# Kernel optimization log

Hardware: AMD Instinct MI355X
Metric: run time of the kernel (lower is better)

The kernel has to match this reference:

```python
import jax, jax.numpy as jnp
import numpy as np

DIM = 1024
B, L = 4, 4096


def setup_inputs() -> dict:
    key = jax.random.key(0)
    ks = jax.random.split(key, 6)
    s = 1.0 / np.sqrt(DIM)
    x = jax.random.normal(ks[0], (B, L, DIM), dtype=jnp.float32)
    Wk = jax.random.uniform(ks[1], (DIM, DIM), jnp.float32, -s, s)
    bk = jax.random.uniform(ks[2], (DIM,), jnp.float32, -s, s)
    Wv = jax.random.uniform(ks[3], (DIM, DIM), jnp.float32, -s, s)
    bv = jax.random.uniform(ks[4], (DIM,), jnp.float32, -s, s)
    ln_g = jnp.ones((DIM,), jnp.float32)
    ln_b = jnp.zeros((DIM,), jnp.float32)
    Wo = jax.random.uniform(ks[5], (DIM, DIM), jnp.float32, -s, s)
    bo = jnp.zeros((DIM,), jnp.float32)
    return {"x": x, "Wk": Wk, "bk": bk, "Wv": Wv, "bv": bv,
            "ln_g": ln_g, "ln_b": ln_b, "Wo": Wo, "bo": bo}


def reference(x, Wk, bk, Wv, bv, ln_g, ln_b, Wo, bo):
    B_, L_, D = x.shape
    # key/value projections (torch Linear: x @ W.T + b)
    keys = x @ Wk.T + bk
    keys = keys / jnp.maximum(jnp.linalg.norm(keys, axis=-1, keepdims=True), 1e-12)
    values = x @ Wv.T + bv
    # circular convolution via FFT: bind keys with values
    Kf = jnp.fft.rfft(keys, axis=-1)
    Vf = jnp.fft.rfft(values, axis=-1)
    bound = jnp.fft.irfft(Kf * Vf, n=D, axis=-1)
    # cumulative holographic memory over sequence
    memory = jnp.cumsum(bound, axis=1)
    # circular correlation (unbind): conj of key spectrum
    Mf = jnp.fft.rfft(memory, axis=-1)
    retrieved = jnp.fft.irfft(Mf * jnp.conj(Kf), n=D, axis=-1)
    # position-dependent normalization: sqrt(1..L)
    norm = jnp.sqrt(jnp.arange(1, L_ + 1, dtype=x.dtype)).reshape(1, L_, 1)
    r = retrieved / norm
    # LayerNorm (eps=1e-5) + output Linear
    mu = jnp.mean(r, axis=-1, keepdims=True)
    var = jnp.var(r, axis=-1, keepdims=True)
    r_ln = (r - mu) * jax.lax.rsqrt(var + 1e-5) * ln_g + ln_b
    return x + (r_ln @ Wo.T + bo)
```

## Files before the change

### kernel.cpp

```cpp
#include <hip/hip_runtime.h>
#include <math.h>

#define B_SZ 4
#define L_SZ 4096
#define D_SZ 1024
#define M_SZ (B_SZ * L_SZ)
#define NBINS 513
#define CCH   (2 * NBINS)
#define TLEN 8
#define NCH  (L_SZ / TLEN)
#define NG   32

typedef short bf16x8 __attribute__((ext_vector_type(8)));
typedef float f32x4  __attribute__((ext_vector_type(4)));
typedef unsigned short us8 __attribute__((ext_vector_type(8)));

#define AS1 __attribute__((address_space(1)))
#define AS3 __attribute__((address_space(3)))

__device__ inline unsigned short f2bf(float f) {
    unsigned int u = __float_as_uint(f);
    u += 0x7fffu + ((u >> 16) & 1u);
    return (unsigned short)(u >> 16);
}

__global__ __launch_bounds__(256) void cast_f32_bf16(
        const float* __restrict__ in, unsigned short* __restrict__ out, int n8) {
    int i = blockIdx.x * 256 + threadIdx.x;
    if (i >= n8) return;
    const float4* p = (const float4*)in + 2 * (size_t)i;
    float4 a = p[0], b = p[1];
    us8 o;
    o[0] = f2bf(a.x); o[1] = f2bf(a.y); o[2] = f2bf(a.z); o[3] = f2bf(a.w);
    o[4] = f2bf(b.x); o[5] = f2bf(b.y); o[6] = f2bf(b.z); o[7] = f2bf(b.w);
    *(us8*)(out + (size_t)i * 8) = o;
}

__global__ __launch_bounds__(256) void cast_w3(
        const float* __restrict__ Wk, const float* __restrict__ Wv,
        const float* __restrict__ Wo,
        unsigned short* __restrict__ WB, unsigned short* __restrict__ Wob, int n8) {
    int i = blockIdx.x * 256 + threadIdx.x;
    if (i >= n8) return;
    const int which = blockIdx.y;
    const float* src = (which == 0) ? Wk : (which == 1) ? Wv : Wo;
    unsigned short* dst = (which == 0) ? WB : (which == 1) ? (WB + D_SZ * D_SZ) : Wob;
    const float4* p = (const float4*)src + 2 * (size_t)i;
    float4 a = p[0], b = p[1];
    us8 o;
    o[0] = f2bf(a.x); o[1] = f2bf(a.y); o[2] = f2bf(a.z); o[3] = f2bf(a.w);
    o[4] = f2bf(b.x); o[5] = f2bf(b.y); o[6] = f2bf(b.z); o[7] = f2bf(b.w);
    *(us8*)(dst + (size_t)i * 8) = o;
}

template<int CNT>
__global__ __launch_bounds__(512, 4) void gemm_mfma(
        const unsigned short* __restrict__ A, const unsigned short* __restrict__ W,
        const float* __restrict__ bias0, const float* __restrict__ bias1,
        const float* __restrict__ resid,
        float* __restrict__ C0, float* __restrict__ C1, int M, int K) {
    __shared__ unsigned short Abuf[3][256 * 32];
    __shared__ unsigned short Bbuf[3][128 * 32];
    const int id   = blockIdx.x;
    const int bx   = (id >> 3) % CNT;
    const int by   = (id & 7) + 8 * (id / (8 * CNT));
    const int tid  = threadIdx.x;
    const int lane = tid & 63;
    const int wid  = tid >> 6;
    const int wr   = wid >> 2;
    const int wc   = wid & 3;
    const int bm   = by * 256;
    const int bn   = bx * 128;

    const int sl = tid >> 3;
    const int sq = (tid & 7) ^ (sl & 7);
    const int srow = 2 * sl + (sq >> 2);
    const int skof = (sq & 3) * 8;
    const unsigned short* Abase = A + (size_t)(bm + srow) * K + skof;
    const unsigned short* Wbase = W + (size_t)(bn + srow) * K + skof;
    const int dstoff = tid * 16;

    auto stage3 = [&](int slot, int kk) {
        __builtin_amdgcn_global_load_lds((const AS1 unsigned int*)(Abase + kk),
            (AS3 unsigned int*)((char*)&Abuf[slot][0] + dstoff), 16, 0, 0);
        __builtin_amdgcn_global_load_lds((const AS1 unsigned int*)(Abase + (size_t)128 * K + kk),
            (AS3 unsigned int*)((char*)&Abuf[slot][128 * 32] + dstoff), 16, 0, 0);
        __builtin_amdgcn_global_load_lds((const AS1 unsigned int*)(Wbase + kk),
            (AS3 unsigned int*)((char*)&Bbuf[slot][0] + dstoff), 16, 0, 0);
    };

    const int fr = lane & 15;
    const int kq = lane >> 4;
    const int rslot = (((((fr & 1) << 2) + kq) ^ ((fr >> 1) & 7)) << 4);
    const int aoff0 = wr * 8192 + (fr >> 1) * 128 + rslot;
    const int boff0 = wc * 2048 + (fr >> 1) * 128 + rslot;

    f32x4 acc[8][2] = {};

    const int nt = K >> 5;
    stage3(0, 0);
    stage3(1, 32);
    asm volatile("s_waitcnt vmcnt(3)" ::: "memory");
    __builtin_amdgcn_s_barrier();
    asm volatile("" ::: "memory");

    int slot = 0, slot2 = 2;
    for (int cur = 0; cur < nt; ++cur) {
        bf16x8 a[8], b[2];
        const char* Ab = (const char*)&Abuf[slot][0];
        const char* Bb = (const char*)&Bbuf[slot][0];
        #pragma unroll
        for (int nf = 0; nf < 2; nf++)
            b[nf] = *(const bf16x8*)(Bb + boff0 + nf * 1024);
        #pragma unroll
        for (int mf = 0; mf < 8; mf++)
            a[mf] = *(const bf16x8*)(Ab + aoff0 + mf * 1024);
        if (cur + 2 < nt) stage3(slot2, (cur + 2) << 5);
        __builtin_amdgcn_s_setprio(1);
        #pragma unroll
        for (int mf = 0; mf < 8; mf++)
            #pragma unroll
            for (int nf = 0; nf < 2; nf++)
                acc[mf][nf] = __builtin_amdgcn_mfma_f32_16x16x32_bf16(
                                  a[mf], b[nf], acc[mf][nf], 0, 0, 0);
        __builtin_amdgcn_s_setprio(0);
        if (cur + 2 < nt) { asm volatile("s_waitcnt vmcnt(3)" ::: "memory"); }
        else              { asm volatile("s_waitcnt vmcnt(0)" ::: "memory"); }
        __builtin_amdgcn_s_barrier();
        asm volatile("" ::: "memory");
        slot  = (slot  == 2) ? 0 : slot  + 1;
        slot2 = (slot2 == 2) ? 0 : slot2 + 1;
    }

    const int col0 = lane & 15;
    const int quad = lane >> 4;
    #pragma unroll
    for (int nf = 0; nf < 2; nf++) {
        const int ng = bn + wc * 32 + nf * 16 + col0;
        const int half = ng >> 10;
        const int n = ng & 1023;
        float* __restrict__ Cp = half ? C1 : C0;
        const float bv = half ? bias1[n] : bias0[n];
        #pragma unroll
        for (int mf = 0; mf < 8; mf++) {
            #pragma unroll
            for (int r = 0; r < 4; r++) {
                const int m = bm + wr * 128 + mf * 16 + quad * 4 + r;
                float v = acc[mf][nf][r] + bv;
                size_t off = (size_t)m * 1024 + n;
                if (resid) v += resid[off];
                Cp[off] = v;
            }
        }
    }
}

#define SWZ(a) ((a) ^ (((a) >> 4) & 15))

struct cplx { float r, i; };
__device__ inline cplx cmul(cplx a, cplx b) {
    return {a.r * b.r - a.i * b.i, a.r * b.i + a.i * b.r};
}

__device__ inline void r4bfly(cplx v[4], float s) {
    cplx t0 {v[0].r + v[2].r, v[0].i + v[2].i};
    cplx t1 {v[0].r - v[2].r, v[0].i - v[2].i};
    cplx t2 {v[1].r + v[3].r, v[1].i + v[3].i};
    cplx t3 {v[1].r - v[3].r, v[1].i - v[3].i};
    cplx j3 {-s * t3.i, s * t3.r};
    v[0] = {t0.r + t2.r, t0.i + t2.i};
    v[2] = {t0.r - t2.r, t0.i - t2.i};
    v[1] = {t1.r + j3.r, t1.i + j3.i};
    v[3] = {t1.r - j3.r, t1.i - j3.i};
}

template<int SIGN>
__device__ inline void make_w1(cplx w1s[4], int tid) {
    const float s = (float)SIGN;
    #pragma unroll
    for (int q = 1; q <= 3; q++) {
        const int Ls = 1 << (2 * q);
        const float ang = s * 1.57079632679489662f * (float)(tid & (Ls - 1)) / (float)Ls;
        float sn, cs; __sincosf(ang, &sn, &cs);
        w1s[q - 1] = {cs, sn};
    }
    float sn, cs;
    __sincosf(s * 1.57079632679489662f * (float)tid / 256.0f, &sn, &cs);
    w1s[3] = {cs, sn};
}

template<int SIGN>
__device__ inline void fft1024_tw(float2* bA, float2* bB, cplx v[4], int tid,
                                  const cplx w1s[4]) {
    const float s = (float)SIGN;
    r4bfly(v, s);
    {
        const int base = tid << 2;
        #pragma unroll
        for (int e = 0; e < 4; e++)
            bA[SWZ(base + e)] = make_float2(v[e].r, v[e].i);
    }
    __syncthreads();
    float2* cur = bA;
    float2* nxt = bB;
    #pragma unroll
    for (int q = 1; q <= 3; q++) {
        const int Ls = 1 << (2 * q);
        #pragma unroll
        for (int k = 0; k < 4; k++) {
            float2 t = cur[SWZ(tid + (k << 8))];
            v[k] = {t.x, t.y};
        }
        const int d = tid & (Ls - 1);
        cplx w1 = w1s[q - 1];
        cplx w2 = cmul(w1, w1);
        cplx w3 = cmul(w2, w1);
        v[1] = cmul(v[1], w1);
        v[2] = cmul(v[2], w2);
        v[3] = cmul(v[3], w3);
        r4bfly(v, s);
        const int base = ((tid >> (2 * q)) << (2 * q + 2)) + d;
        #pragma unroll
        for (int e = 0; e < 4; e++)
            nxt[SWZ(base + (e << (2 * q)))] = make_float2(v[e].r, v[e].i);
        float2* tmp = cur; cur = nxt; nxt = tmp;
        __syncthreads();
    }
    #pragma unroll
    for (int k = 0; k < 4; k++) {
        float2 t = cur[SWZ(tid + (k << 8))];
        v[k] = {t.x, t.y};
    }
    {
        cplx w1 = w1s[3];
        cplx w2 = cmul(w1, w1);
        cplx w3 = cmul(w2, w1);
        v[1] = cmul(v[1], w1);
        v[2] = cmul(v[2], w2);
        v[3] = cmul(v[3], w3);
        r4bfly(v, s);
    }
}

__global__ __launch_bounds__(256) void bind_cum_kernel(
        float* __restrict__ KIO, const float* __restrict__ V,
        float* __restrict__ P, float* __restrict__ totals) {
    __shared__ float2 bA[1024], bB[1024];
    __shared__ float red[4];
    const int blk = blockIdx.x;
    const int tid = threadIdx.x;
    const int wv  = tid >> 6;
    const int ln  = tid & 63;
    const size_t tok0 = (size_t)blk * TLEN;

    cplx w1s[4];
    make_w1<-1>(w1s, tid);

    float r0r = 0.f, r0i = 0.f, r1r = 0.f, r1i = 0.f, r2r = 0.f, r2i = 0.f;

    float kvC[4], vvC[4];
    {
        const float* krow = KIO + tok0 * D_SZ;
        const float* vrow = V   + tok0 * D_SZ;
        #pragma unroll
        for (int k = 0; k < 4; k++) {
            kvC[k] = krow[tid + (k << 8)];
            vvC[k] = vrow[tid + (k << 8)];
        }
    }

    for (int tk = 0; tk < TLEN; ++tk) {
        const size_t token = tok0 + tk;
        float* krow = KIO + token * D_SZ;

        float ss = 0.f;
        #pragma unroll
        for (int k = 0; k < 4; k++) ss += kvC[k] * kvC[k];
        #pragma unroll
        for (int m = 1; m < 64; m <<= 1) ss += __shfl_xor(ss, m, 64);
        if (ln == 0) red[wv] = ss;
        __syncthreads();
        const float scale = 1.0f /
            fmaxf(sqrtf(red[0] + red[1] + red[2] + red[3]), 1e-12f);

        cplx z[4];
        #pragma unroll
        for (int k = 0; k < 4; k++) z[k] = {kvC[k] * scale, vvC[k]};

        if (tk + 1 < TLEN) {
            const float* krowN = KIO + (token + 1) * D_SZ;
            const float* vrowN = V   + (token + 1) * D_SZ;
            #pragma unroll
            for (int k = 0; k < 4; k++) {
                kvC[k] = krowN[tid + (k << 8)];
                vvC[k] = vrowN[tid + (k << 8)];
            }
        }

        fft1024_tw<-1>(bA, bB, z, tid, w1s);

        #pragma unroll
        for (int e = 0; e < 4; e++)
            bA[SWZ(tid + (e << 8))] = make_float2(z[e].r, z[e].i);
        __syncthreads();

        float2* Po = (float2*)(P + token * CCH);
        auto procbin = [&](int bin, float& rr, float& ri) {
            float2 Zb = bA[SWZ(bin)];
            float2 Zm = bA[SWZ((1024 - bin) & 1023)];
            float ar = 0.5f * (Zb.x + Zm.x);
            float ai = 0.5f * (Zb.y - Zm.y);
            float br = 0.5f * (Zb.y + Zm.y);
            float bi = 0.5f * (Zm.x - Zb.x);
            rr += ar * br - ai * bi;
            ri += ar * bi + ai * br;
            Po[bin] = make_float2(rr, ri);
            if (bin == 0)        krow[0] = ar;
            else if (bin == 512) krow[1] = ar;
            else { krow[2 * bin] = ar; krow[2 * bin + 1] = ai; }
        };
        procbin(tid,       r0r, r0i);
        procbin(tid + 256, r1r, r1i);
        if (tid == 0) procbin(512, r2r, r2i);
    }

    float* trow = totals + (size_t)blk * CCH;
    trow[2 * tid]             = r0r;  trow[2 * tid + 1]         = r0i;
    trow[2 * (tid + 256)]     = r1r;  trow[2 * (tid + 256) + 1] = r1i;
    if (tid == 0) { trow[1024] = r2r; trow[1025] = r2i; }
}

__global__ __launch_bounds__(256) void scan_s1(
        float* __restrict__ totals, float* __restrict__ gt) {
    const int c = blockIdx.x * 256 + threadIdx.x;
    if (c >= CCH) return;
    const int g = blockIdx.y;
    const int b = blockIdx.z;
    float run = 0.f;
    #pragma unroll
    for (int i = 0; i < 16; i++) {
        size_t idx = ((size_t)(b * NCH + g * 16 + i)) * CCH + c;
        float v = totals[idx];
        totals[idx] = run;
        run += v;
    }
    gt[((size_t)(b * NG + g)) * CCH + c] = run;
}

__global__ __launch_bounds__(256) void scan_s2(float* __restrict__ gt) {
    const int c = blockIdx.x * 256 + threadIdx.x;
    if (c >= CCH) return;
    const int b = blockIdx.y;
    float run = 0.f;
    #pragma unroll
    for (int g = 0; g < NG; g++) {
        size_t idx = ((size_t)(b * NG + g)) * CCH + c;
        float v = gt[idx];
        gt[idx] = run;
        run += v;
    }
}

__global__ __launch_bounds__(256) void unbind4_ln_kernel(
        const float* __restrict__ P, const float* __restrict__ totals,
        const float* __restrict__ gt, const float* __restrict__ KF,
        const float* __restrict__ ln_g, const float* __restrict__ ln_b,
        unsigned short* __restrict__ RLNb) {
    __shared__ float2 bA[1024], bB[1024];
    __shared__ float2 offsh[NBINS];
    __shared__ float red[16];
    const int blk = blockIdx.x;
    const int tid = threadIdx.x;
    const int wv  = tid >> 6;
    const int ln  = tid & 63;
    const size_t tok0 = (size_t)blk * TLEN;
    const int bidx  = (int)(tok0 >> 12);
    const int t0    = (int)(tok0 & (L_SZ - 1));
    const int chunk = t0 >> 3;

    {
        const float2* off2 = (const float2*)(totals + (size_t)(bidx * NCH + chunk) * CCH);
        const float2* gof2 = (const float2*)(gt + (size_t)(bidx * NG + (chunk >> 4)) * CCH);
        auto ldo = [&](int bin) {
            float2 o = off2[bin], g = gof2[bin];
            offsh[bin] = make_float2(o.x + g.x, o.y + g.y);
        };
        ldo(tid); ldo(tid + 256);
        if (tid == 0) ldo(512);
    }

    cplx w1s[4];
    make_w1<1>(w1s, tid);

    float gv[4], bev[4];
    #pragma unroll
    for (int e = 0; e < 4; e++) {
        gv[e]  = ln_g[tid + (e << 8)];
        bev[e] = ln_b[tid + (e << 8)];
    }
    __syncthreads();

    for (int p = 0; p < 4; ++p) {
        const size_t ta = tok0 + 2 * p, tb = ta + 1;
        const float2* Sa2 = (const float2*)(P + ta * CCH);
        const float2* Sb2 = (const float2*)(P + tb * CCH);
        const float*  Ka  = KF + ta * D_SZ;
        const float*  Kb  = KF + tb * D_SZ;

        auto zc = [&](int bin, const float2* S2, const float* kf, float2 og) {
            float kr, ki;
            if (bin == 0)        { kr = kf[0]; ki = 0.f; }
            else if (bin == 512) { kr = kf[1]; ki = 0.f; }
            else { float2 k2 = *(const float2*)(kf + 2 * bin); kr = k2.x; ki = k2.y; }
            float2 s2 = S2[bin];
            float sr = s2.x + og.x, si = s2.y + og.y;
            return make_float2(sr * kr + si * ki, si * kr - sr * ki);
        };
        auto fill = [&](int bin) {
            float2 og = offsh[bin];
            float2 Za = zc(bin, Sa2, Ka, og);
            float2 Zb = zc(bin, Sb2, Kb, og);
            bA[SWZ(bin)] = make_float2(Za.x - Zb.y, Za.y + Zb.x);
            if (bin != 0 && bin != 512)
                bA[SWZ(1024 - bin)] = make_float2(Za.x + Zb.y, Zb.x - Za.y);
        };
        fill(tid);
        fill(tid + 256);
        if (tid == 0) fill(512);
        __syncthreads();

        cplx z[4];
        #pragma unroll
        for (int k = 0; k < 4; k++) {
            float2 c = bA[SWZ(tid + (k << 8))];
            z[k] = {c.x, c.y};
        }
        __syncthreads();
        fft1024_tw<1>(bA, bB, z, tid, w1s);

        const int t_a = t0 + 2 * p;
        const float sa = (1.0f / 1024.0f) * rsqrtf((float)(t_a + 1));
        const float sb = (1.0f / 1024.0f) * rsqrtf((float)(t_a + 2));
        float ra[4], rb[4];
        float s1a = 0.f, s2a = 0.f, s1b = 0.f, s2b = 0.f;
        #pragma unroll
        for (int e = 0; e < 4; e++) {
            ra[e] = z[e].r * sa;
            rb[e] = z[e].i * sb;
            s1a += ra[e]; s2a += ra[e] * ra[e];
            s1b += rb[e]; s2b += rb[e] * rb[e];
        }
        #pragma unroll
        for (int m = 1; m < 64; m <<= 1) {
            s1a += __shfl_xor(s1a, m, 64);
            s2a += __shfl_xor(s2a, m, 64);
            s1b += __shfl_xor(s1b, m, 64);
            s2b += __shfl_xor(s2b, m, 64);
        }
        if (ln == 0) {
            red[wv] = s1a; red[4 + wv] = s2a; red[8 + wv] = s1b; red[12 + wv] = s2b;
        }
        __syncthreads();
        const float S1a = red[0] + red[1] + red[2] + red[3];
        const float S2a = red[4] + red[5] + red[6] + red[7];
        const float S1b = red[8] + red[9] + red[10] + red[11];
        const float S2b = red[12] + red[13] + red[14] + red[15];
        const float mua = S1a * (1.0f / 1024.0f);
        const float vara = S2a * (1.0f / 1024.0f) - mua * mua;
        const float rsa = rsqrtf(vara + 1e-5f);
        const float mub = S1b * (1.0f / 1024.0f);
        const float varb = S2b * (1.0f / 1024.0f) - mub * mub;
        const float rsb = rsqrtf(varb + 1e-5f);

        unsigned short* outA = RLNb + ta * D_SZ;
        unsigned short* outB = RLNb + tb * D_SZ;
        #pragma unroll
        for (int e = 0; e < 4; e++) {
            const int d = tid + (e << 8);
            outA[d] = f2bf((ra[e] - mua) * rsa * gv[e] + bev[e]);
            outB[d] = f2bf((rb[e] - mub) * rsb * gv[e] + bev[e]);
        }
        __syncthreads();
    }
}

extern "C" void kernel_launch(void* const* d_in, const int* in_sizes, int n_in,
                              void* d_out, int out_size, void* d_ws, size_t ws_size,
                              hipStream_t stream) {
    (void)in_sizes; (void)n_in; (void)out_size; (void)ws_size;
    const float* x    = (const float*)d_in[0];
    const float* Wk   = (const float*)d_in[1];
    const float* bk   = (const float*)d_in[2];
    const float* Wv   = (const float*)d_in[3];
    const float* bv   = (const float*)d_in[4];
    const float* ln_g = (const float*)d_in[5];
    const float* ln_b = (const float*)d_in[6];
    const float* Wo   = (const float*)d_in[7];
    const float* bo   = (const float*)d_in[8];
    float* out = (float*)d_out;

    char* w = (char*)d_ws;
    float* Kraw   = (float*)w;  w += (size_t)M_SZ * D_SZ * 4;
    float* V      = (float*)w;  w += (size_t)M_SZ * D_SZ * 4;
    float* P      = (float*)w;  w += (size_t)M_SZ * CCH * 4;
    unsigned short* xb  = (unsigned short*)w;  w += (size_t)M_SZ * D_SZ * 2;
    unsigned short* WB  = (unsigned short*)w;  w += (size_t)2 * D_SZ * D_SZ * 2;
    unsigned short* Wob = (unsigned short*)w;  w += (size_t)D_SZ * D_SZ * 2;
    unsigned short* RLNb = (unsigned short*)V;
    float* totals = (float*)xb;
    float* gt     = (float*)xb + (size_t)B_SZ * NCH * CCH;

    const int n8x = M_SZ * D_SZ / 8;
    const int n8w = D_SZ * D_SZ / 8;
    cast_f32_bf16<<<n8x / 256, 256, 0, stream>>>(x, xb, n8x);
    dim3 wgrid(n8w / 256, 3);
    cast_w3<<<wgrid, 256, 0, stream>>>(Wk, Wv, Wo, WB, Wob, n8w);

    gemm_mfma<16><<<(M_SZ / 256) * 16, 512, 0, stream>>>(
        xb, WB, bk, bv, nullptr, Kraw, V, M_SZ, D_SZ);

    bind_cum_kernel<<<M_SZ / TLEN, 256, 0, stream>>>(Kraw, V, P, totals);

    dim3 g1((CCH + 255) / 256, NG, B_SZ);
    scan_s1<<<g1, 256, 0, stream>>>(totals, gt);
    dim3 g2((CCH + 255) / 256, B_SZ);
    scan_s2<<<g2, 256, 0, stream>>>(gt);

    unbind4_ln_kernel<<<M_SZ / TLEN, 256, 0, stream>>>(
        P, totals, gt, Kraw, ln_g, ln_b, RLNb);

    gemm_mfma<8><<<(M_SZ / 256) * 8, 512, 0, stream>>>(
        RLNb, Wob, bo, bo, x, out, out, M_SZ, D_SZ);
}
```

Before: 391.2 us.

## Store K/V projections and partial spectra intermediates in bf16

The projection GEMM now writes K and V in bf16 rather than fp32. The bind kernel reads them as bf16 and writes its partial-sum spectra P and the key spectra in bf16, and the unbind kernel reads them back as bf16. This roughly halves the global-memory traffic between the GEMM, bind and unbind stages. In exchange, precision drops in the intermediates, including the prefix-sum partials, which can raise numerical error.

```diff
diff --git a/kernel.cpp b/kernel.cpp
--- a/kernel.cpp
+++ b/kernel.cpp
@@ -22,6 +22,9 @@
     unsigned int u = __float_as_uint(f);
     u += 0x7fffu + ((u >> 16) & 1u);
     return (unsigned short)(u >> 16);
+}
+__device__ inline float bf2f(unsigned short u) {
+    return __uint_as_float(((unsigned int)u) << 16);
 }
 
 __global__ __launch_bounds__(256) void cast_f32_bf16(
@@ -53,12 +56,12 @@
     *(us8*)(dst + (size_t)i * 8) = o;
 }
 
-template<int CNT>
+template<int CNT, bool OBF16>
 __global__ __launch_bounds__(512, 4) void gemm_mfma(
         const unsigned short* __restrict__ A, const unsigned short* __restrict__ W,
         const float* __restrict__ bias0, const float* __restrict__ bias1,
         const float* __restrict__ resid,
-        float* __restrict__ C0, float* __restrict__ C1, int M, int K) {
+        void* __restrict__ C0v, void* __restrict__ C1v, int M, int K) {
     __shared__ unsigned short Abuf[3][256 * 32];
     __shared__ unsigned short Bbuf[3][128 * 32];
     const int id   = blockIdx.x;
@@ -139,8 +142,8 @@
         const int ng = bn + wc * 32 + nf * 16 + col0;
         const int half = ng >> 10;
         const int n = ng & 1023;
-        float* __restrict__ Cp = half ? C1 : C0;
         const float bv = half ? bias1[n] : bias0[n];
+        void* Cv = half ? C1v : C0v;
         #pragma unroll
         for (int mf = 0; mf < 8; mf++) {
             #pragma unroll
@@ -148,8 +151,12 @@
                 const int m = bm + wr * 128 + mf * 16 + quad * 4 + r;
                 float v = acc[mf][nf][r] + bv;
                 size_t off = (size_t)m * 1024 + n;
-                if (resid) v += resid[off];
-                Cp[off] = v;
+                if constexpr (OBF16) {
+                    ((unsigned short*)Cv)[off] = f2bf(v);
+                } else {
+                    if (resid) v += resid[off];
+                    ((float*)Cv)[off] = v;
+                }
             }
         }
     }
@@ -243,8 +250,8 @@
 }
 
 __global__ __launch_bounds__(256) void bind_cum_kernel(
-        float* __restrict__ KIO, const float* __restrict__ V,
-        float* __restrict__ P, float* __restrict__ totals) {
+        unsigned short* __restrict__ KIO, const unsigned short* __restrict__ Vb,
+        unsigned short* __restrict__ P, float* __restrict__ totals) {
     __shared__ float2 bA[1024], bB[1024];
     __shared__ float red[4];
     const int blk = blockIdx.x;
@@ -260,18 +267,18 @@
 
     float kvC[4], vvC[4];
     {
-        const float* krow = KIO + tok0 * D_SZ;
-        const float* vrow = V   + tok0 * D_SZ;
+        const unsigned short* krow = KIO + tok0 * D_SZ;
+        const unsigned short* vrow = Vb  + tok0 * D_SZ;
         #pragma unroll
         for (int k = 0; k < 4; k++) {
-            kvC[k] = krow[tid + (k << 8)];
-            vvC[k] = vrow[tid + (k << 8)];
+            kvC[k] = bf2f(krow[tid + (k << 8)]);
+            vvC[k] = bf2f(vrow[tid + (k << 8)]);
         }
     }
 
     for (int tk = 0; tk < TLEN; ++tk) {
         const size_t token = tok0 + tk;
-        float* krow = KIO + token * D_SZ;
+        unsigned short* krow = KIO + token * D_SZ;
 
         float ss = 0.f;
         #pragma unroll
@@ -288,12 +295,12 @@
         for (int k = 0; k < 4; k++) z[k] = {kvC[k] * scale, vvC[k]};
 
         if (tk + 1 < TLEN) {
-            const float* krowN = KIO + (token + 1) * D_SZ;
-            const float* vrowN = V   + (token + 1) * D_SZ;
+            const unsigned short* krowN = KIO + (token + 1) * D_SZ;
+            const unsigned short* vrowN = Vb  + (token + 1) * D_SZ;
             #pragma unroll
             for (int k = 0; k < 4; k++) {
-                kvC[k] = krowN[tid + (k << 8)];
-                vvC[k] = vrowN[tid + (k << 8)];
+                kvC[k] = bf2f(krowN[tid + (k << 8)]);
+                vvC[k] = bf2f(vrowN[tid + (k << 8)]);
             }
         }
 
@@ -304,7 +311,7 @@
             bA[SWZ(tid + (e << 8))] = make_float2(z[e].r, z[e].i);
         __syncthreads();
 
-        float2* Po = (float2*)(P + token * CCH);
+        ushort2* Po = (ushort2*)(P + token * CCH);
         auto procbin = [&](int bin, float& rr, float& ri) {
             float2 Zb = bA[SWZ(bin)];
             float2 Zm = bA[SWZ((1024 - bin) & 1023)];
@@ -314,10 +321,14 @@
             float bi = 0.5f * (Zm.x - Zb.x);
             rr += ar * br - ai * bi;
             ri += ar * bi + ai * br;
-            Po[bin] = make_float2(rr, ri);
-            if (bin == 0)        krow[0] = ar;
-            else if (bin == 512) krow[1] = ar;
-            else { krow[2 * bin] = ar; krow[2 * bin + 1] = ai; }
+            ushort2 pv; pv.x = f2bf(rr); pv.y = f2bf(ri);
+            Po[bin] = pv;
+            if (bin == 0)        krow[0] = f2bf(ar);
+            else if (bin == 512) krow[1] = f2bf(ar);
+            else {
+                ushort2 kv2; kv2.x = f2bf(ar); kv2.y = f2bf(ai);
+                *(ushort2*)(krow + 2 * bin) = kv2;
+            }
         };
         procbin(tid,       r0r, r0i);
         procbin(tid + 256, r1r, r1i);
@@ -362,8 +373,8 @@
 }
 
 __global__ __launch_bounds__(256) void unbind4_ln_kernel(
-        const float* __restrict__ P, const float* __restrict__ totals,
-        const float* __restrict__ gt, const float* __restrict__ KF,
+        const unsigned short* __restrict__ P, const float* __restrict__ totals,
+        const float* __restrict__ gt, const unsigned short* __restrict__ KF,
         const float* __restrict__ ln_g, const float* __restrict__ ln_b,
         unsigned short* __restrict__ RLNb) {
     __shared__ float2 bA[1024], bB[1024];
@@ -402,18 +413,21 @@
 
     for (int p = 0; p < 4; ++p) {
         const size_t ta = tok0 + 2 * p, tb = ta + 1;
-        const float2* Sa2 = (const float2*)(P + ta * CCH);
-        const float2* Sb2 = (const float2*)(P + tb * CCH);
-        const float*  Ka  = KF + ta * D_SZ;
-        const float*  Kb  = KF + tb * D_SZ;
-
-        auto zc = [&](int bin, const float2* S2, const float* kf, float2 og) {
+        const ushort2* Sa2 = (const ushort2*)(P + ta * CCH);
+        const ushort2* Sb2 = (const ushort2*)(P + tb * CCH);
+        const unsigned short* Ka = KF + ta * D_SZ;
+        const unsigned short* Kb = KF + tb * D_SZ;
+
+        auto zc = [&](int bin, const ushort2* S2, const unsigned short* kf, float2 og) {
             float kr, ki;
-            if (bin == 0)        { kr = kf[0]; ki = 0.f; }
-            else if (bin == 512) { kr = kf[1]; ki = 0.f; }
-            else { float2 k2 = *(const float2*)(kf + 2 * bin); kr = k2.x; ki = k2.y; }
-            float2 s2 = S2[bin];
-            float sr = s2.x + og.x, si = s2.y + og.y;
+            if (bin == 0)        { kr = bf2f(kf[0]); ki = 0.f; }
+            else if (bin == 512) { kr = bf2f(kf[1]); ki = 0.f; }
+            else {
+                ushort2 k2 = *(const ushort2*)(kf + 2 * bin);
+                kr = bf2f(k2.x); ki = bf2f(k2.y);
+            }
+            ushort2 s2 = S2[bin];
+            float sr = bf2f(s2.x) + og.x, si = bf2f(s2.y) + og.y;
             return make_float2(sr * kr + si * ki, si * kr - sr * ki);
         };
         auto fill = [&](int bin) {
@@ -500,13 +514,13 @@
     float* out = (float*)d_out;
 
     char* w = (char*)d_ws;
-    float* Kraw   = (float*)w;  w += (size_t)M_SZ * D_SZ * 4;
-    float* V      = (float*)w;  w += (size_t)M_SZ * D_SZ * 4;
-    float* P      = (float*)w;  w += (size_t)M_SZ * CCH * 4;
+    unsigned short* Kb  = (unsigned short*)w;  w += (size_t)M_SZ * D_SZ * 2;
+    unsigned short* Vb  = (unsigned short*)w;  w += (size_t)M_SZ * D_SZ * 2;
+    unsigned short* Pb  = (unsigned short*)w;  w += (size_t)M_SZ * CCH * 2;
     unsigned short* xb  = (unsigned short*)w;  w += (size_t)M_SZ * D_SZ * 2;
     unsigned short* WB  = (unsigned short*)w;  w += (size_t)2 * D_SZ * D_SZ * 2;
     unsigned short* Wob = (unsigned short*)w;  w += (size_t)D_SZ * D_SZ * 2;
-    unsigned short* RLNb = (unsigned short*)V;
+    unsigned short* RLNb = Vb;
     float* totals = (float*)xb;
     float* gt     = (float*)xb + (size_t)B_SZ * NCH * CCH;
 
@@ -516,10 +530,10 @@
     dim3 wgrid(n8w / 256, 3);
     cast_w3<<<wgrid, 256, 0, stream>>>(Wk, Wv, Wo, WB, Wob, n8w);
 
-    gemm_mfma<16><<<(M_SZ / 256) * 16, 512, 0, stream>>>(
-        xb, WB, bk, bv, nullptr, Kraw, V, M_SZ, D_SZ);
-
-    bind_cum_kernel<<<M_SZ / TLEN, 256, 0, stream>>>(Kraw, V, P, totals);
+    gemm_mfma<16, true><<<(M_SZ / 256) * 16, 512, 0, stream>>>(
+        xb, WB, bk, bv, nullptr, Kb, Vb, M_SZ, D_SZ);
+
+    bind_cum_kernel<<<M_SZ / TLEN, 256, 0, stream>>>(Kb, Vb, Pb, totals);
 
     dim3 g1((CCH + 255) / 256, NG, B_SZ);
     scan_s1<<<g1, 256, 0, stream>>>(totals, gt);
@@ -527,8 +541,8 @@
     scan_s2<<<g2, 256, 0, stream>>>(gt);
 
     unbind4_ln_kernel<<<M_SZ / TLEN, 256, 0, stream>>>(
-        P, totals, gt, Kraw, ln_g, ln_b, RLNb);
-
-    gemm_mfma<8><<<(M_SZ / 256) * 8, 512, 0, stream>>>(
+        Pb, totals, gt, Kb, ln_g, ln_b, RLNb);
+
+    gemm_mfma<8, false><<<(M_SZ / 256) * 8, 512, 0, stream>>>(
         RLNb, Wob, bo, bo, x, out, out, M_SZ, D_SZ);
 }
```

New measurement: 389.7 us. Within noise of the previous version (-0.4%).
